# Kernel optimization log

Hardware: AMD Instinct MI355X
Metric: run time of the kernel (lower is better)

## Reference

```python
import jax, jax.numpy as jnp
import numpy as np

D, NH, HD, NL, NP, DFF = 256, 8, 32, 4, 4, 1024
B, LQ = 16, 900
SHAPES = np.array([[100, 100], [50, 50], [25, 25], [13, 13]], dtype=np.int64)
_AREAS = SHAPES[:, 0] * SHAPES[:, 1]
LSI = np.concatenate([[0], np.cumsum(_AREAS)[:-1]]).astype(np.int64)
S = int(_AREAS.sum())  # 13294


def setup_inputs() -> dict:
    key = jax.random.key(0)
    ki = iter(jax.random.split(key, 40))
    def nrm(shape, s=1.0):
        return jax.random.normal(next(ki), shape, jnp.float32) * s
    p = dict(
        tgt=nrm((B, LQ, D)),
        query_pos=nrm((B, LQ, D)) * 0.1,
        reference_points=jax.random.uniform(next(ki), (B, LQ, NL, 2), jnp.float32),
        src=nrm((B, S, D)),
        src_spatial_shapes=SHAPES,
        level_start_index=LSI,
        src_padding_mask=np.zeros((B, S), dtype=bool),
        Wq=nrm((D, D), 0.02), bq=jnp.zeros((D,)),
        Wk=nrm((D, D), 0.02), bk=jnp.zeros((D,)),
        Wv=nrm((D, D), 0.02), bv=jnp.zeros((D,)),
        Wo=nrm((D, D), 0.02), bo=jnp.zeros((D,)),
        g2=jnp.ones((D,)), be2=jnp.zeros((D,)),
        Woff=nrm((D, NH * NL * NP * 2), 0.02),
        boff=jax.random.uniform(next(ki), (NH * NL * NP * 2,), jnp.float32, -0.5, 0.5),
        Waw=nrm((D, NH * NL * NP), 0.02), baw=jnp.zeros((NH * NL * NP,)),
        Wval=nrm((D, D), 0.02), bval=jnp.zeros((D,)),
        Wout=nrm((D, D), 0.02), bout=jnp.zeros((D,)),
        g1=jnp.ones((D,)), be1=jnp.zeros((D,)),
        W1f=nrm((D, DFF), 0.02), b1f=jnp.zeros((DFF,)),
        W2f=nrm((DFF, D), 0.02), b2f=jnp.zeros((D,)),
        g3=jnp.ones((D,)), be3=jnp.zeros((D,)),
    )
    return p


def layernorm(x, g, b):
    m = jnp.mean(x, -1, keepdims=True)
    v = jnp.var(x, -1, keepdims=True)
    return (x - m) * jax.lax.rsqrt(v + 1e-5) * g + b


def reference(tgt, query_pos, reference_points, src, src_spatial_shapes,
              level_start_index, src_padding_mask,
              Wq, bq, Wk, bk, Wv, bv, Wo, bo, g2, be2,
              Woff, boff, Waw, baw, Wval, bval, Wout, bout, g1, be1,
              W1f, b1f, W2f, b2f, g3, be3):
    Bq, Lq, _ = tgt.shape
    # ---- self-attention (q = k = tgt + pos, v = tgt), dropout in eval = identity
    q = tgt + query_pos
    qh = (q @ Wq + bq).reshape(Bq, Lq, NH, HD)
    kh = (q @ Wk + bk).reshape(Bq, Lq, NH, HD)
    vh = (tgt @ Wv + bv).reshape(Bq, Lq, NH, HD)
    att = jax.nn.softmax(jnp.einsum('bqhd,bkhd->bhqk', qh, kh) / np.sqrt(HD), axis=-1)
    sa = jnp.einsum('bhqk,bkhd->bqhd', att, vh).reshape(Bq, Lq, D) @ Wo + bo
    tgt = layernorm(tgt + sa, g2, be2)
    # ---- multi-scale deformable cross-attention
    query = tgt + query_pos
    value = src @ Wval + bval
    value = jnp.where(jnp.asarray(src_padding_mask)[..., None], 0.0, value)
    value = value.reshape(Bq, -1, NH, HD)
    off = (query @ Woff + boff).reshape(Bq, Lq, NH, NL, NP, 2)
    aw = jax.nn.softmax((query @ Waw + baw).reshape(Bq, Lq, NH, NL * NP), axis=-1)
    aw = aw.reshape(Bq, Lq, NH, NL, NP)
    ss = np.asarray(src_spatial_shapes)
    lsi = np.asarray(level_start_index)
    norm = jnp.asarray(ss[:, ::-1].astype(np.float32))  # (W, H) per level
    # sampling locations in [0,1]: [B, Lq, NH, NL, NP, 2]
    loc = reference_points[:, :, None, :, None, :] + off / norm[None, None, None, :, None, :]
    out = jnp.zeros((Bq, NH, Lq, HD), value.dtype)
    for l in range(NL):
        Hc, Wc = int(ss[l, 0]), int(ss[l, 1])
        v2 = value[:, lsi[l]:lsi[l] + Hc * Wc].transpose(0, 2, 1, 3)  # [B, NH, H*W, HD]
        x = loc[:, :, :, l, :, 0] * Wc - 0.5  # [B, Lq, NH, NP] (align_corners=False)
        y = loc[:, :, :, l, :, 1] * Hc - 0.5
        x0 = jnp.floor(x); y0 = jnp.floor(y)
        lx = x - x0; ly = y - y0
        x0i = x0.astype(jnp.int32); y0i = y0.astype(jnp.int32)
        samp = jnp.zeros((Bq, NH, Lq * NP, HD), value.dtype)
        for dy, dx, w in ((0, 0, (1 - ly) * (1 - lx)), (0, 1, (1 - ly) * lx),
                          (1, 0, ly * (1 - lx)), (1, 1, ly * lx)):
            xi = x0i + dx; yi = y0i + dy
            valid = (xi >= 0) & (xi < Wc) & (yi >= 0) & (yi < Hc)  # zero padding
            idx = jnp.clip(yi, 0, Hc - 1) * Wc + jnp.clip(xi, 0, Wc - 1)
            idx2 = idx.transpose(0, 2, 1, 3).reshape(Bq, NH, Lq * NP)
            g = jnp.take_along_axis(v2, idx2[..., None], axis=2)  # [B, NH, Lq*NP, HD]
            wv = (w * valid).transpose(0, 2, 1, 3).reshape(Bq, NH, Lq * NP)
            samp = samp + wv[..., None] * g
        samp = samp.reshape(Bq, NH, Lq, NP, HD)
        out = out + jnp.einsum('bqhp,bhqpd->bhqd', aw[:, :, :, l, :], samp)
    ca = out.transpose(0, 2, 1, 3).reshape(Bq, Lq, D) @ Wout + bout
    tgt = layernorm(tgt + ca, g1, be1)
    # ---- FFN
    ff = jax.nn.relu(tgt @ W1f + b1f) @ W2f + b2f
    return layernorm(tgt + ff, g3, be3)
```

## Files before the change

kernel.cpp:

```cpp
#include <hip/hip_runtime.h>
#include <math.h>

#define DD 256
#define NH 8
#define HD 32
#define NL 4
#define NP 4
#define DFF 1024
#define BB 16
#define LQ 900
#define S_TOT 13294

#define M1   (BB * LQ)
#define MP1  14464
#define MV   (BB * S_TOT)
#define MPV  212736

typedef unsigned short u16;
typedef unsigned int   u32;
typedef __attribute__((ext_vector_type(8))) short s8v;
typedef __attribute__((ext_vector_type(4))) float f32x4;

__constant__ int c_H[NL]    = {100, 50, 25, 13};
__constant__ int c_W[NL]    = {100, 50, 25, 13};
__constant__ int c_base[NL] = {0, 10000, 12500, 13125};

__device__ __forceinline__ float b2f(u16 u) {
    return __uint_as_float(((u32)u) << 16);
}
__device__ __forceinline__ u16 f2b(float f) {
    u32 x = __float_as_uint(f);
    u32 r = x + 0x7fffu + ((x >> 16) & 1u);
    return (u16)(r >> 16);
}
__device__ __forceinline__ u32 pk2(float a, float b) {
    return (u32)f2b(a) | ((u32)f2b(b) << 16);
}
__device__ __forceinline__ void gload16(const u16* g, u16* ldsbase) {
    __builtin_amdgcn_global_load_lds(
        (const __attribute__((address_space(1))) unsigned int*)(const void*)g,
        (__attribute__((address_space(3))) unsigned int*)(void*)ldsbase,
        16, 0, 0);
}

#define OFF_QK   0
#define OFF_V    131072
#define OFF_O    196608
#define OFF_VAL  262144
#define OFF_OUT  327680
#define OFF_OA   393216
#define OFF_F1   491520
#define OFF_F2   753664
#define WTS_TOT  1015808

__global__ __launch_bounds__(256)
void prep_kernel(const float* __restrict__ Wq, const float* __restrict__ Wk,
                 const float* __restrict__ Wv, const float* __restrict__ Wo,
                 const float* __restrict__ Wval, const float* __restrict__ Wout,
                 const float* __restrict__ Woff, const float* __restrict__ Waw,
                 const float* __restrict__ W1f, const float* __restrict__ W2f,
                 const float* __restrict__ pbq, const float* __restrict__ pbk,
                 const float* __restrict__ boff, const float* __restrict__ baw,
                 u16* __restrict__ WTS, float* __restrict__ bqk, float* __restrict__ boa)
{
    int t = blockIdx.x;
    if (t >= 992) {
        if (t == 992) {
            for (int i = threadIdx.x; i < 512; i += 256)
                bqk[i] = (i < 256) ? pbq[i] : pbk[i - 256];
        } else {
            for (int i = threadIdx.x; i < 384; i += 256)
                boa[i] = (i < 256) ? boff[i] : baw[i - 256];
        }
        return;
    }
    const float* src; u16* dst; int K, N, tt;
    if (t < 448) {
        int wsel = t >> 6; tt = t & 63;
        const float* srcs[7] = {Wq, Wk, Wv, Wo, Wval, Wout, Woff};
        const int   offs[7]  = {OFF_QK, OFF_QK + 65536, OFF_V, OFF_O, OFF_VAL, OFF_OUT, OFF_OA};
        src = srcs[wsel]; dst = WTS + offs[wsel]; K = 256; N = 256;
    } else if (t < 480) {
        tt = t - 448; src = Waw; dst = WTS + OFF_OA + 65536; K = 256; N = 128;
    } else if (t < 736) {
        tt = t - 480; src = W1f; dst = WTS + OFF_F1; K = 256; N = 1024;
    } else {
        tt = t - 736; src = W2f; dst = WTS + OFF_F2; K = 1024; N = 256;
    }
    int nt = N / 32;
    int n0 = (tt % nt) * 32, k0 = (tt / nt) * 32;

    __shared__ float tb[32][33];
    int tx = threadIdx.x & 31, ty = threadIdx.x >> 5;
    #pragma unroll
    for (int i = 0; i < 4; ++i) {
        int k = ty + i * 8;
        tb[k][tx] = src[(size_t)(k0 + k) * N + n0 + tx];
    }
    __syncthreads();
    #pragma unroll
    for (int i = 0; i < 4; ++i) {
        int n = ty + i * 8;
        dst[(size_t)(n0 + n) * K + k0 + tx] = f2b(tb[tx][n]);
    }
}

__global__ __launch_bounds__(256)
void acvt2_kernel(const float* __restrict__ tgt, const float* __restrict__ qpos,
                  u16* __restrict__ B0, u16* __restrict__ B1)
{
    int i8 = blockIdx.x * 256 + threadIdx.x;
    int row = i8 >> 5;
    uint4 o0, o1;
    if (row < M1) {
        const float4* tp = (const float4*)(tgt + (size_t)i8 * 8);
        const float4* pp = (const float4*)(qpos + (size_t)i8 * 8);
        float4 t0 = tp[0], t1 = tp[1], p0 = pp[0], p1 = pp[1];
        o1.x = pk2(t0.x, t0.y); o1.y = pk2(t0.z, t0.w);
        o1.z = pk2(t1.x, t1.y); o1.w = pk2(t1.z, t1.w);
        o0.x = pk2(t0.x + p0.x, t0.y + p0.y); o0.y = pk2(t0.z + p0.z, t0.w + p0.w);
        o0.z = pk2(t1.x + p1.x, t1.y + p1.y); o0.w = pk2(t1.z + p1.z, t1.w + p1.w);
    } else {
        o0.x = o0.y = o0.z = o0.w = 0;
        o1 = o0;
    }
    ((uint4*)B0)[i8] = o0;
    ((uint4*)B1)[i8] = o1;
}

template<int BNT, int AF32, int OUTBF, int RELU>
__global__ __launch_bounds__(256)
void mgemm(const void* __restrict__ Av, const u16* __restrict__ Bt,
           const float* __restrict__ bias, void* __restrict__ Cv,
           int K, int N, int Mreal)
{
    constexpr int MF = (BNT == 128) ? 4 : 2;
    __shared__ u16 Asu[128 * 32];
    __shared__ u16 Bsu[BNT * 32];

    int tid = threadIdx.x;
    int w = tid >> 6, l = tid & 63;
    int mbase = (BNT == 128) ? (w >> 1) * 64 : w * 32;
    int nbase = (BNT == 128) ? (w & 1) * 64 : 0;
    long m0 = (long)blockIdx.y * 128;
    int n0 = blockIdx.x * BNT;

    f32x4 acc[MF][4];
    #pragma unroll
    for (int i = 0; i < MF; ++i)
        #pragma unroll
        for (int j = 0; j < 4; ++j) {
            acc[i][j][0] = 0.f; acc[i][j][1] = 0.f;
            acc[i][j][2] = 0.f; acc[i][j][3] = 0.f;
        }

    int lr = l & 15, lk = (l >> 4) * 8;
    int srow = l >> 2;
    int scol = (l & 3) * 8;

    for (int k0 = 0; k0 < K; k0 += 32) {
        if (BNT == 128) {
            #pragma unroll
            for (int j = 0; j < 2; ++j) {
                int row = w * 32 + j * 16;
                gload16(Bt + (size_t)(n0 + row + srow) * K + k0 + scol, &Bsu[row * 32]);
            }
        } else {
            int row = w * 16;
            gload16(Bt + (size_t)(n0 + row + srow) * K + k0 + scol, &Bsu[row * 32]);
        }
        if (AF32) {
            const float* A = (const float*)Av;
            int c = tid;
            #pragma unroll
            for (int it = 0; it < 4; ++it) {
                int row = c >> 3, col = (c & 7) * 4;
                long gr = m0 + row;
                if (gr >= Mreal) gr = Mreal - 1;
                float4 v = *(const float4*)(A + gr * K + k0 + col);
                ushort4 o;
                o.x = f2b(v.x); o.y = f2b(v.y); o.z = f2b(v.z); o.w = f2b(v.w);
                ((ushort4*)Asu)[c] = o;
                c += 256;
            }
        } else {
            const u16* A = (const u16*)Av;
            #pragma unroll
            for (int j = 0; j < 2; ++j) {
                int row = w * 32 + j * 16;
                gload16(A + (m0 + row + srow) * (long)K + k0 + scol, &Asu[row * 32]);
            }
        }
        __syncthreads();
        s8v af[MF], bf[4];
        #pragma unroll
        for (int mi = 0; mi < MF; ++mi)
            af[mi] = *(const s8v*)(Asu + (mbase + mi * 16 + lr) * 32 + lk);
        #pragma unroll
        for (int nj = 0; nj < 4; ++nj)
            bf[nj] = *(const s8v*)(Bsu + (nbase + nj * 16 + lr) * 32 + lk);
        #pragma unroll
        for (int mi = 0; mi < MF; ++mi)
            #pragma unroll
            for (int nj = 0; nj < 4; ++nj)
                acc[mi][nj] = __builtin_amdgcn_mfma_f32_16x16x32_bf16(
                    af[mi], bf[nj], acc[mi][nj], 0, 0, 0);
        __syncthreads();
    }

    int lq = l >> 4;
    #pragma unroll
    for (int nj = 0; nj < 4; ++nj) {
        int col = n0 + nbase + nj * 16 + lr;
        float bv = bias[col];
        #pragma unroll
        for (int mi = 0; mi < MF; ++mi) {
            #pragma unroll
            for (int r = 0; r < 4; ++r) {
                long row = m0 + mbase + mi * 16 + lq * 4 + r;
                float v = acc[mi][nj][r] + bv;
                if (RELU) v = fmaxf(v, 0.f);
                if (OUTBF) ((u16*)Cv)[row * N + col] = f2b(v);
                else       ((float*)Cv)[row * N + col] = v;
            }
        }
    }
}

#define QT 64
#define KT2 64
#define KSP 48
#define VSP 40
#define PSP 72
__global__ __launch_bounds__(256)
void mattn(const u16* __restrict__ qk, const u16* __restrict__ vh,
           u16* __restrict__ sa)
{
    __shared__ u16 Ks[KT2][KSP];
    __shared__ u32 Vt32[32][VSP];
    __shared__ u16 Ps[4][16][PSP];

    int tid = threadIdx.x;
    int w = tid >> 6, l = tid & 63;
    int lr = l & 15, hi = l >> 4;
    int b = blockIdx.x >> 3, h = blockIdx.x & 7;
    int q0 = blockIdx.y * QT + w * 16;

    s8v qf;
    {
        s8v raw = *(const s8v*)(qk + ((size_t)(b * LQ + q0 + lr) * 512) + h * HD + hi * 8);
        #pragma unroll
        for (int j = 0; j < 8; ++j)
            raw[j] = (short)f2b(b2f((u16)raw[j]) * 0.17677669529663687f);
        qf = raw;
    }

    f32x4 o0 = {0.f,0.f,0.f,0.f}, o1 = {0.f,0.f,0.f,0.f};
    float lrun[4] = {0.f,0.f,0.f,0.f};

    const u16* kbase = qk + (size_t)b * LQ * 512 + 256 + h * HD;
    const u16* vbase = vh + (size_t)b * LQ * 256 + h * HD;

    int krow = tid >> 2, kc8 = (tid & 3) * 8;
    int k2 = tid & 31, d0 = (tid >> 5) * 4;

    for (int kb = 0; kb < LQ; kb += KT2) {
        int gk = kb + krow;        if (gk >= LQ) gk = LQ - 1;
        int gv0 = kb + 2 * k2;     if (gv0 >= LQ) gv0 = LQ - 1;
        int gv1 = kb + 2 * k2 + 1; if (gv1 >= LQ) gv1 = LQ - 1;
        uint4 kv = *(const uint4*)(kbase + (size_t)gk * 512 + kc8);
        uint2 va = *(const uint2*)(vbase + (size_t)gv0 * 256 + d0);
        uint2 vb = *(const uint2*)(vbase + (size_t)gv1 * 256 + d0);
        __syncthreads();
        *(uint4*)(&Ks[krow][kc8]) = kv;
        Vt32[d0 + 0][k2] = (va.x & 0xffffu)      | (vb.x << 16);
        Vt32[d0 + 1][k2] = (va.x >> 16)          | (vb.x & 0xffff0000u);
        Vt32[d0 + 2][k2] = (va.y & 0xffffu)      | (vb.y << 16);
        Vt32[d0 + 3][k2] = (va.y >> 16)          | (vb.y & 0xffff0000u);
        __syncthreads();

        f32x4 s[4];
        #pragma unroll
        for (int kk = 0; kk < 4; ++kk) {
            s8v bk = *(const s8v*)(&Ks[kk * 16 + lr][hi * 8]);
            f32x4 z = {0.f,0.f,0.f,0.f};
            s[kk] = __builtin_amdgcn_mfma_f32_16x16x32_bf16(qf, bk, z, 0, 0, 0);
        }
        if (kb + KT2 > LQ) {
            #pragma unroll
            for (int kk = 0; kk < 4; ++kk)
                if (kb + kk * 16 + lr >= LQ) {
                    s[kk][0] = -1e30f; s[kk][1] = -1e30f;
                    s[kk][2] = -1e30f; s[kk][3] = -1e30f;
                }
        }

        #pragma unroll
        for (int r = 0; r < 4; ++r) {
            float p0 = __expf(s[0][r]);
            float p1 = __expf(s[1][r]);
            float p2 = __expf(s[2][r]);
            float p3 = __expf(s[3][r]);
            lrun[r] += (p0 + p1) + (p2 + p3);
            int qr = hi * 4 + r;
            Ps[w][qr][lr]      = f2b(p0);
            Ps[w][qr][16 + lr] = f2b(p1);
            Ps[w][qr][32 + lr] = f2b(p2);
            Ps[w][qr][48 + lr] = f2b(p3);
        }

        s8v ap0  = *(const s8v*)(&Ps[w][lr][hi * 8]);
        s8v ap1  = *(const s8v*)(&Ps[w][lr][32 + hi * 8]);
        s8v bv00 = *(const s8v*)(&Vt32[lr][hi * 4]);
        s8v bv10 = *(const s8v*)(&Vt32[lr][16 + hi * 4]);
        s8v bv01 = *(const s8v*)(&Vt32[16 + lr][hi * 4]);
        s8v bv11 = *(const s8v*)(&Vt32[16 + lr][16 + hi * 4]);
        o0 = __builtin_amdgcn_mfma_f32_16x16x32_bf16(ap0, bv00, o0, 0, 0, 0);
        o0 = __builtin_amdgcn_mfma_f32_16x16x32_bf16(ap1, bv10, o0, 0, 0, 0);
        o1 = __builtin_amdgcn_mfma_f32_16x16x32_bf16(ap0, bv01, o1, 0, 0, 0);
        o1 = __builtin_amdgcn_mfma_f32_16x16x32_bf16(ap1, bv11, o1, 0, 0, 0);
    }

    #pragma unroll
    for (int r = 0; r < 4; ++r) {
        float ps = lrun[r];
        ps += __shfl_xor(ps, 1);
        ps += __shfl_xor(ps, 2);
        ps += __shfl_xor(ps, 4);
        ps += __shfl_xor(ps, 8);
        int q = q0 + hi * 4 + r;
        if (q < LQ) {
            float inv = 1.f / ps;
            u16* op = sa + (size_t)(b * LQ + q) * DD + h * HD;
            op[lr]      = f2b(o0[r] * inv);
            op[16 + lr] = f2b(o1[r] * inv);
        }
    }
}

__global__ __launch_bounds__(256)
void ln_kernel(const float* __restrict__ x, const u16* __restrict__ y,
               const float* __restrict__ g, const float* __restrict__ be,
               float* __restrict__ out, const float* __restrict__ pos,
               u16* __restrict__ bfout, int M)
{
    int wave = threadIdx.x >> 6;
    int lane = threadIdx.x & 63;
    int row = blockIdx.x * 4 + wave;
    if (row >= M) return;
    float4 xv = ((const float4*)(x + (size_t)row * DD))[lane];
    ushort4 yv = ((const ushort4*)(y + (size_t)row * DD))[lane];
    float v[4] = {xv.x + b2f(yv.x), xv.y + b2f(yv.y),
                  xv.z + b2f(yv.z), xv.w + b2f(yv.w)};
    float s = v[0] + v[1] + v[2] + v[3];
    float sq = v[0]*v[0] + v[1]*v[1] + v[2]*v[2] + v[3]*v[3];
    for (int o = 32; o; o >>= 1) {
        s += __shfl_xor(s, o);
        sq += __shfl_xor(sq, o);
    }
    float mean = s * (1.f / DD);
    float var = sq * (1.f / DD) - mean * mean;
    float r = rsqrtf(var + 1e-5f);
    float4 gv = ((const float4*)g)[lane];
    float4 bv = ((const float4*)be)[lane];
    float4 ov;
    ov.x = (v[0] - mean) * r * gv.x + bv.x;
    ov.y = (v[1] - mean) * r * gv.y + bv.y;
    ov.z = (v[2] - mean) * r * gv.z + bv.z;
    ov.w = (v[3] - mean) * r * gv.w + bv.w;
    ((float4*)(out + (size_t)row * DD))[lane] = ov;
    if (bfout) {
        float4 pv = make_float4(0.f, 0.f, 0.f, 0.f);
        if (pos) pv = ((const float4*)(pos + (size_t)row * DD))[lane];
        ushort4 bo;
        bo.x = f2b(ov.x + pv.x); bo.y = f2b(ov.y + pv.y);
        bo.z = f2b(ov.z + pv.z); bo.w = f2b(ov.w + pv.w);
        ((ushort4*)(bfout + (size_t)row * DD))[lane] = bo;
    }
}

__global__ __launch_bounds__(256)
void sample_kernel(const float* __restrict__ offaw, const float* __restrict__ refp,
                   const u16* __restrict__ value, u16* __restrict__ out)
{
    __shared__ float2 sPW[2][128][4];
    int t = threadIdx.x;
    int sub = t >> 7;
    int bq = blockIdx.x * 2 + sub;
    int b = bq / LQ;

    {
        int pt = t & 127;
        int h = pt >> 4, j = pt & 15, l = j >> 2, p = j & 3;
        const float* row = offaw + (size_t)bq * 384;
        float lg = row[256 + h * 16 + j];
        float mx = lg;
        mx = fmaxf(mx, __shfl_xor(mx, 1));
        mx = fmaxf(mx, __shfl_xor(mx, 2));
        mx = fmaxf(mx, __shfl_xor(mx, 4));
        mx = fmaxf(mx, __shfl_xor(mx, 8));
        float e = __expf(lg - mx);
        float se = e;
        se += __shfl_xor(se, 1);
        se += __shfl_xor(se, 2);
        se += __shfl_xor(se, 4);
        se += __shfl_xor(se, 8);
        float aw = e / se;

        float ox = row[h * 32 + l * 8 + p * 2 + 0];
        float oy = row[h * 32 + l * 8 + p * 2 + 1];
        int Hc = c_H[l], Wc = c_W[l];
        float x = refp[(size_t)bq * 8 + l * 2 + 0] * Wc + ox - 0.5f;
        float y = refp[(size_t)bq * 8 + l * 2 + 1] * Hc + oy - 0.5f;
        float x0f = floorf(x), y0f = floorf(y);
        float lx = x - x0f, ly = y - y0f;
        int x0 = (int)x0f, y0 = (int)y0f;
        int vb = (b * S_TOT + c_base[l]) * 128;
        #pragma unroll
        for (int c = 0; c < 4; ++c) {
            int dy = c >> 1, dx = c & 1;
            int xi = x0 + dx, yi = y0 + dy;
            bool ok = (xi >= 0) & (xi < Wc) & (yi >= 0) & (yi < Hc);
            float wgt = (dy ? ly : 1.f - ly) * (dx ? lx : 1.f - lx) * aw;
            float2 pw;
            pw.x = __int_as_float(ok ? vb + (yi * Wc + xi) * 128 : 0);
            pw.y = ok ? wgt : 0.f;
            sPW[sub][pt][c] = pw;
        }
    }
    __syncthreads();

    {
        int s = t & 127;
        int h = s >> 4, d2 = s & 15;
        const u32* v32 = (const u32*)value;
        int lane = h * 16 + d2;
        float a0 = 0.f, a1 = 0.f;
        #pragma unroll
        for (int j = 0; j < 16; ++j) {
            #pragma unroll
            for (int c = 0; c < 4; ++c) {
                float2 pw = sPW[sub][h * 16 + j][c];
                u32 pv = v32[__float_as_int(pw.x) + lane];
                a0 += pw.y * __uint_as_float(pv << 16);
                a1 += pw.y * __uint_as_float(pv & 0xffff0000u);
            }
        }
        *(u32*)(out + (size_t)bq * DD + h * 32 + d2 * 2) = pk2(a0, a1);
    }
}

extern "C" void kernel_launch(void* const* d_in, const int* in_sizes, int n_in,
                              void* d_out, int out_size, void* d_ws, size_t ws_size,
                              hipStream_t stream)
{
    const float* tgt  = (const float*)d_in[0];
    const float* qpos = (const float*)d_in[1];
    const float* refp = (const float*)d_in[2];
    const float* src  = (const float*)d_in[3];
    const float* Wq  = (const float*)d_in[7];
    const float* pbq = (const float*)d_in[8];
    const float* Wk  = (const float*)d_in[9];
    const float* pbk = (const float*)d_in[10];
    const float* Wv  = (const float*)d_in[11];
    const float* pbv = (const float*)d_in[12];
    const float* Wo  = (const float*)d_in[13];
    const float* pbo = (const float*)d_in[14];
    const float* g2  = (const float*)d_in[15];
    const float* be2 = (const float*)d_in[16];
    const float* Woff = (const float*)d_in[17];
    const float* boff = (const float*)d_in[18];
    const float* Waw  = (const float*)d_in[19];
    const float* baw  = (const float*)d_in[20];
    const float* Wval = (const float*)d_in[21];
    const float* bval = (const float*)d_in[22];
    const float* Wout = (const float*)d_in[23];
    const float* bout = (const float*)d_in[24];
    const float* g1   = (const float*)d_in[25];
    const float* be1  = (const float*)d_in[26];
    const float* W1f  = (const float*)d_in[27];
    const float* b1f  = (const float*)d_in[28];
    const float* W2f  = (const float*)d_in[29];
    const float* b2f_ = (const float*)d_in[30];
    const float* g3   = (const float*)d_in[31];
    const float* be3  = (const float*)d_in[32];

    char* base = (char*)d_ws;
    size_t off = 0;
    auto alloc = [&](size_t bytes) -> void* {
        void* p = base + off;
        off = (off + bytes + 255) & ~(size_t)255;
        return p;
    };
    const size_t AB = (size_t)MP1 * DD * sizeof(u16);
    u16* B0  = (u16*)alloc(AB);
    u16* B1  = (u16*)alloc(AB);
    u16* BQK = (u16*)alloc((size_t)MP1 * 512 * sizeof(u16));
    u16* B4  = (u16*)alloc(AB);
    u16* TMPB= (u16*)alloc(AB);
    u16* FFH = (u16*)alloc((size_t)MP1 * DFF * sizeof(u16));
    u16* VAL = (u16*)alloc((size_t)MPV * DD * sizeof(u16));
    float* F0 = (float*)alloc((size_t)MP1 * 384 * sizeof(float));
    float* F2 = (float*)alloc((size_t)MP1 * DD * sizeof(float));
    float* F3 = (float*)alloc((size_t)MP1 * DD * sizeof(float));
    u16* WTS = (u16*)alloc((size_t)WTS_TOT * sizeof(u16));
    float* bqk = (float*)alloc(512 * sizeof(float));
    float* boa = (float*)alloc(384 * sizeof(float));

    dim3 blk(256);

    prep_kernel<<<dim3(994), blk, 0, stream>>>(
        Wq, Wk, Wv, Wo, Wval, Wout, Woff, Waw, W1f, W2f,
        pbq, pbk, boff, baw, WTS, bqk, boa);

    const int MT = MP1 / 128;
    const dim3 gval(2, MPV / 128);
    const dim3 g512b(8,  MT);
    const dim3 g256b(4,  MT);
    const dim3 g384b(6,  MT);
    const dim3 g1kb(16,  MT);

    acvt2_kernel<<<dim3(MP1 * 32 / 256), blk, 0, stream>>>(tgt, qpos, B0, B1);
    mgemm<64,0,1,0><<<g512b, blk, 0, stream>>>(B0, WTS + OFF_QK, bqk, BQK, DD, 512, M1);
    mgemm<64,0,1,0><<<g256b, blk, 0, stream>>>(B1, WTS + OFF_V, pbv, B4, DD, DD, M1);
    mattn<<<dim3(BB * NH, (LQ + QT - 1) / QT), blk, 0, stream>>>(BQK, B4, B0);
    mgemm<64,0,1,0><<<g256b, blk, 0, stream>>>(B0, WTS + OFF_O, pbo, TMPB, DD, DD, M1);
    ln_kernel<<<dim3(M1 / 4), blk, 0, stream>>>(tgt, TMPB, g2, be2, F2, qpos, B1, M1);

    mgemm<128,1,1,0><<<gval, blk, 0, stream>>>(src, WTS + OFF_VAL, bval, VAL, DD, DD, MV);
    mgemm<64,0,0,0><<<g384b, blk, 0, stream>>>(B1, WTS + OFF_OA, boa, F0, DD, 384, M1);
    sample_kernel<<<dim3(M1 / 2), blk, 0, stream>>>(F0, refp, VAL, B4);
    mgemm<64,0,1,0><<<g256b, blk, 0, stream>>>(B4, WTS + OFF_OUT, bout, TMPB, DD, DD, M1);
    ln_kernel<<<dim3(M1 / 4), blk, 0, stream>>>(F2, TMPB, g1, be1, F3, nullptr, B1, M1);

    mgemm<64,0,1,1><<<g1kb, blk, 0, stream>>>(B1, WTS + OFF_F1, b1f, FFH, DD, DFF, M1);
    mgemm<64,0,1,0><<<g256b, blk, 0, stream>>>(FFH, WTS + OFF_F2, b2f_, TMPB, DFF, DD, M1);
    ln_kernel<<<dim3(M1 / 4), blk, 0, stream>>>(F3, TMPB, g3, be3, (float*)d_out, nullptr, nullptr, M1);
}
```

Baseline: 332.5 us.

## Fuse pos-add conversion into QKV GEMMs and restructure deformable sampling kernel

Removes the separate fp32-to-bf16 conversion kernel and instead lets the Q/K and V GEMMs read fp32 tgt directly, adding query_pos on the fly for the Q/K projection. The sampling kernel now handles one query per 256-thread block. Each thread gathers 8-byte (4 bf16) value chunks over a quarter of the sampling points, and the four partial sums are reduced through shared memory. This cuts one launch and one intermediate round trip through memory, and widens the gathers. In exchange the fp32 A-tile load plus pos add happens inside the GEMMs, and the sampler gains an extra sync and reduction step.

```diff
diff --git a/kernel.cpp b/kernel.cpp
--- a/kernel.cpp
+++ b/kernel.cpp
@@ -105,34 +105,11 @@
     }
 }
 
-__global__ __launch_bounds__(256)
-void acvt2_kernel(const float* __restrict__ tgt, const float* __restrict__ qpos,
-                  u16* __restrict__ B0, u16* __restrict__ B1)
-{
-    int i8 = blockIdx.x * 256 + threadIdx.x;
-    int row = i8 >> 5;
-    uint4 o0, o1;
-    if (row < M1) {
-        const float4* tp = (const float4*)(tgt + (size_t)i8 * 8);
-        const float4* pp = (const float4*)(qpos + (size_t)i8 * 8);
-        float4 t0 = tp[0], t1 = tp[1], p0 = pp[0], p1 = pp[1];
-        o1.x = pk2(t0.x, t0.y); o1.y = pk2(t0.z, t0.w);
-        o1.z = pk2(t1.x, t1.y); o1.w = pk2(t1.z, t1.w);
-        o0.x = pk2(t0.x + p0.x, t0.y + p0.y); o0.y = pk2(t0.z + p0.z, t0.w + p0.w);
-        o0.z = pk2(t1.x + p1.x, t1.y + p1.y); o0.w = pk2(t1.z + p1.z, t1.w + p1.w);
-    } else {
-        o0.x = o0.y = o0.z = o0.w = 0;
-        o1 = o0;
-    }
-    ((uint4*)B0)[i8] = o0;
-    ((uint4*)B1)[i8] = o1;
-}
-
 template<int BNT, int AF32, int OUTBF, int RELU>
 __global__ __launch_bounds__(256)
 void mgemm(const void* __restrict__ Av, const u16* __restrict__ Bt,
            const float* __restrict__ bias, void* __restrict__ Cv,
-           int K, int N, int Mreal)
+           int K, int N, int Mreal, const float* __restrict__ pos)
 {
     constexpr int MF = (BNT == 128) ? 4 : 2;
     __shared__ u16 Asu[128 * 32];
@@ -178,6 +155,10 @@
                 long gr = m0 + row;
                 if (gr >= Mreal) gr = Mreal - 1;
                 float4 v = *(const float4*)(A + gr * K + k0 + col);
+                if (pos) {
+                    float4 p = *(const float4*)(pos + gr * K + k0 + col);
+                    v.x += p.x; v.y += p.y; v.z += p.z; v.w += p.w;
+                }
                 ushort4 o;
                 o.x = f2b(v.x); o.y = f2b(v.y); o.z = f2b(v.z); o.w = f2b(v.w);
                 ((ushort4*)Asu)[c] = o;
@@ -383,14 +364,15 @@
 void sample_kernel(const float* __restrict__ offaw, const float* __restrict__ refp,
                    const u16* __restrict__ value, u16* __restrict__ out)
 {
-    __shared__ float2 sPW[2][128][4];
+    __shared__ float2 sPW[128][4];
+    __shared__ float4 sPart[4][64];
+
     int t = threadIdx.x;
-    int sub = t >> 7;
-    int bq = blockIdx.x * 2 + sub;
+    int bq = blockIdx.x;
     int b = bq / LQ;
 
-    {
-        int pt = t & 127;
+    if (t < 128) {
+        int pt = t;
         int h = pt >> 4, j = pt & 15, l = j >> 2, p = j & 3;
         const float* row = offaw + (size_t)bq * 384;
         float lg = row[256 + h * 16 + j];
@@ -415,7 +397,7 @@
         float x0f = floorf(x), y0f = floorf(y);
         float lx = x - x0f, ly = y - y0f;
         int x0 = (int)x0f, y0 = (int)y0f;
-        int vb = (b * S_TOT + c_base[l]) * 128;
+        int vb = (b * S_TOT + c_base[l]) * 64;
         #pragma unroll
         for (int c = 0; c < 4; ++c) {
             int dy = c >> 1, dx = c & 1;
@@ -423,30 +405,63 @@
             bool ok = (xi >= 0) & (xi < Wc) & (yi >= 0) & (yi < Hc);
             float wgt = (dy ? ly : 1.f - ly) * (dx ? lx : 1.f - lx) * aw;
             float2 pw;
-            pw.x = __int_as_float(ok ? vb + (yi * Wc + xi) * 128 : 0);
+            pw.x = __int_as_float(ok ? vb + (yi * Wc + xi) * 64 : 0);
             pw.y = ok ? wgt : 0.f;
-            sPW[sub][pt][c] = pw;
+            sPW[pt][c] = pw;
         }
     }
     __syncthreads();
 
     {
-        int s = t & 127;
-        int h = s >> 4, d2 = s & 15;
-        const u32* v32 = (const u32*)value;
-        int lane = h * 16 + d2;
-        float a0 = 0.f, a1 = 0.f;
-        #pragma unroll
-        for (int j = 0; j < 16; ++j) {
-            #pragma unroll
-            for (int c = 0; c < 4; ++c) {
-                float2 pw = sPW[sub][h * 16 + j][c];
-                u32 pv = v32[__float_as_int(pw.x) + lane];
-                a0 += pw.y * __uint_as_float(pv << 16);
-                a1 += pw.y * __uint_as_float(pv & 0xffff0000u);
-            }
-        }
-        *(u32*)(out + (size_t)bq * DD + h * 32 + d2 * 2) = pk2(a0, a1);
+        int jq = t >> 6, h = (t >> 3) & 7, d4 = t & 7;
+        const uint2* v64 = (const uint2*)value;
+        int lane = h * 8 + d4;
+        float a0 = 0.f, a1 = 0.f, a2 = 0.f, a3 = 0.f;
+        #pragma unroll
+        for (int jj = 0; jj < 4; ++jj) {
+            int pt = h * 16 + jq * 4 + jj;
+            float2 pw0 = sPW[pt][0];
+            float2 pw1 = sPW[pt][1];
+            float2 pw2 = sPW[pt][2];
+            float2 pw3 = sPW[pt][3];
+            uint2 g0 = v64[__float_as_int(pw0.x) + lane];
+            uint2 g1 = v64[__float_as_int(pw1.x) + lane];
+            uint2 g2 = v64[__float_as_int(pw2.x) + lane];
+            uint2 g3 = v64[__float_as_int(pw3.x) + lane];
+            a0 += pw0.y * __uint_as_float(g0.x << 16);
+            a1 += pw0.y * __uint_as_float(g0.x & 0xffff0000u);
+            a2 += pw0.y * __uint_as_float(g0.y << 16);
+            a3 += pw0.y * __uint_as_float(g0.y & 0xffff0000u);
+            a0 += pw1.y * __uint_as_float(g1.x << 16);
+            a1 += pw1.y * __uint_as_float(g1.x & 0xffff0000u);
+            a2 += pw1.y * __uint_as_float(g1.y << 16);
+            a3 += pw1.y * __uint_as_float(g1.y & 0xffff0000u);
+            a0 += pw2.y * __uint_as_float(g2.x << 16);
+            a1 += pw2.y * __uint_as_float(g2.x & 0xffff0000u);
+            a2 += pw2.y * __uint_as_float(g2.y << 16);
+            a3 += pw2.y * __uint_as_float(g2.y & 0xffff0000u);
+            a0 += pw3.y * __uint_as_float(g3.x << 16);
+            a1 += pw3.y * __uint_as_float(g3.x & 0xffff0000u);
+            a2 += pw3.y * __uint_as_float(g3.y << 16);
+            a3 += pw3.y * __uint_as_float(g3.y & 0xffff0000u);
+        }
+        sPart[jq][h * 8 + d4] = make_float4(a0, a1, a2, a3);
+    }
+    __syncthreads();
+
+    if (t < 64) {
+        float4 p0 = sPart[0][t];
+        float4 p1 = sPart[1][t];
+        float4 p2 = sPart[2][t];
+        float4 p3 = sPart[3][t];
+        float a0 = (p0.x + p1.x) + (p2.x + p3.x);
+        float a1 = (p0.y + p1.y) + (p2.y + p3.y);
+        float a2 = (p0.z + p1.z) + (p2.z + p3.z);
+        float a3 = (p0.w + p1.w) + (p2.w + p3.w);
+        uint2 o;
+        o.x = pk2(a0, a1);
+        o.y = pk2(a2, a3);
+        *(uint2*)(out + (size_t)bq * DD + t * 4) = o;
     }
 }
 
@@ -520,20 +535,19 @@
     const dim3 g384b(6,  MT);
     const dim3 g1kb(16,  MT);
 
-    acvt2_kernel<<<dim3(MP1 * 32 / 256), blk, 0, stream>>>(tgt, qpos, B0, B1);
-    mgemm<64,0,1,0><<<g512b, blk, 0, stream>>>(B0, WTS + OFF_QK, bqk, BQK, DD, 512, M1);
-    mgemm<64,0,1,0><<<g256b, blk, 0, stream>>>(B1, WTS + OFF_V, pbv, B4, DD, DD, M1);
+    mgemm<64,1,1,0><<<g512b, blk, 0, stream>>>(tgt, WTS + OFF_QK, bqk, BQK, DD, 512, M1, qpos);
+    mgemm<64,1,1,0><<<g256b, blk, 0, stream>>>(tgt, WTS + OFF_V, pbv, B4, DD, DD, M1, nullptr);
     mattn<<<dim3(BB * NH, (LQ + QT - 1) / QT), blk, 0, stream>>>(BQK, B4, B0);
-    mgemm<64,0,1,0><<<g256b, blk, 0, stream>>>(B0, WTS + OFF_O, pbo, TMPB, DD, DD, M1);
+    mgemm<64,0,1,0><<<g256b, blk, 0, stream>>>(B0, WTS + OFF_O, pbo, TMPB, DD, DD, M1, nullptr);
     ln_kernel<<<dim3(M1 / 4), blk, 0, stream>>>(tgt, TMPB, g2, be2, F2, qpos, B1, M1);
 
-    mgemm<128,1,1,0><<<gval, blk, 0, stream>>>(src, WTS + OFF_VAL, bval, VAL, DD, DD, MV);
-    mgemm<64,0,0,0><<<g384b, blk, 0, stream>>>(B1, WTS + OFF_OA, boa, F0, DD, 384, M1);
-    sample_kernel<<<dim3(M1 / 2), blk, 0, stream>>>(F0, refp, VAL, B4);
-    mgemm<64,0,1,0><<<g256b, blk, 0, stream>>>(B4, WTS + OFF_OUT, bout, TMPB, DD, DD, M1);
+    mgemm<128,1,1,0><<<gval, blk, 0, stream>>>(src, WTS + OFF_VAL, bval, VAL, DD, DD, MV, nullptr);
+    mgemm<64,0,0,0><<<g384b, blk, 0, stream>>>(B1, WTS + OFF_OA, boa, F0, DD, 384, M1, nullptr);
+    sample_kernel<<<dim3(M1), blk, 0, stream>>>(F0, refp, VAL, B4);
+    mgemm<64,0,1,0><<<g256b, blk, 0, stream>>>(B4, WTS + OFF_OUT, bout, TMPB, DD, DD, M1, nullptr);
     ln_kernel<<<dim3(M1 / 4), blk, 0, stream>>>(F2, TMPB, g1, be1, F3, nullptr, B1, M1);
 
-    mgemm<64,0,1,1><<<g1kb, blk, 0, stream>>>(B1, WTS + OFF_F1, b1f, FFH, DD, DFF, M1);
-    mgemm<64,0,1,0><<<g256b, blk, 0, stream>>>(FFH, WTS + OFF_F2, b2f_, TMPB, DFF, DD, M1);
+    mgemm<64,0,1,1><<<g1kb, blk, 0, stream>>>(B1, WTS + OFF_F1, b1f, FFH, DD, DFF, M1, nullptr);
+    mgemm<64,0,1,0><<<g256b, blk, 0, stream>>>(FFH, WTS + OFF_F2, b2f_, TMPB, DFF, DD, M1, nullptr);
     ln_kernel<<<dim3(M1 / 4), blk, 0, stream>>>(F3, TMPB, g3, be3, (float*)d_out, nullptr, nullptr, M1);
 }
```

Result: slower. 385.8 us (+16.0%).
